# Kernel tuning notes

Measured on AMD Instinct MI355X. Metric: run time of the kernel, lower is better.

The kernel has to match this reference:

```python
import jax, jax.numpy as jnp
import numpy as np

N_TOK, TOKDIM = 2048, 1024
NHEADS, KDIM = 16, 64


def setup_inputs() -> dict:
    key = jax.random.key(0)
    kg, kk, kq = jax.random.split(key, 3)
    g = jax.random.normal(kg, (N_TOK, TOKDIM), dtype=jnp.float32)
    # params use normal(stddev=0.002) init, as in the flax module
    Wk = 0.002 * jax.random.normal(kk, (NHEADS, KDIM, TOKDIM), dtype=jnp.float32)
    Wq = 0.002 * jax.random.normal(kq, (NHEADS, KDIM, TOKDIM), dtype=jnp.float32)
    return {"g": g, "Wk": Wk, "Wq": Wq}


def reference(g, Wk, Wq):
    """manual_grad of the attention energy: returns d(energy)/dg, shape [n, d]."""
    H, Z, D = Wk.shape
    betas = jnp.full((H,), 1.0, dtype=g.dtype) / jnp.sqrt(jnp.asarray(Z, g.dtype))
    K = jnp.einsum('hzd,kd->khz', Wk, g)   # [n,h,z]
    Q = jnp.einsum('hzd,qd->qhz', Wq, g)   # [n,h,z]
    F1 = jnp.einsum('hzd,khz->khd', Wq, K)  # [n,h,d]
    F2 = jnp.einsum('hzd,qhz->qhd', Wk, Q)  # [n,h,d]
    A1 = jnp.einsum('h,khz,qhz->hqk', betas, K, Q)  # [h,q,k] scores
    A2 = jax.nn.softmax(A1, -1)
    T1 = -jnp.einsum('khd,hqk->qd', F1, A2)
    T2 = -jnp.einsum('qhd,hqk->kd', F2, A2)
    return T1 + T2
```

## Files before the change

### kernel.cpp

```cpp
#include <hip/hip_runtime.h>
#include <stdint.h>

#define NT 2048
#define TD 1024
#define NH 16
static constexpr float SCL = 0.18033688011112042f;

typedef __attribute__((ext_vector_type(8))) short bf16x8;
typedef __attribute__((ext_vector_type(4))) float f32x4;
typedef __attribute__((address_space(3))) uint32_t lds_u32;
typedef __attribute__((address_space(1))) uint32_t glb_u32;

__device__ __forceinline__ float bf2f(unsigned short u){
  union { uint32_t u32; float f; } v; v.u32 = ((uint32_t)u) << 16; return v.f;
}
__device__ __forceinline__ unsigned short f2bf(float f){
  union { float f; uint32_t u; } v; v.f = f;
  uint32_t r = v.u + 0x7fffu + ((v.u >> 16) & 1u);
  return (unsigned short)(r >> 16);
}
__device__ __forceinline__ bf16x8 ld8(const unsigned short* base, int row, int kc){
  return *(const bf16x8*)((const char*)base + row*128 + ((kc ^ (row & 7)) << 4));
}
__device__ __forceinline__ bf16x8 ld16(const unsigned short* base, int row, int kc){
  return *(const bf16x8*)((const char*)base + row*256 + ((kc ^ (row & 15)) << 4));
}
template<int N> __device__ __forceinline__ void wait_vm_lgkm0(){
  if constexpr (N == 0)      asm volatile("s_waitcnt vmcnt(0) lgkmcnt(0)" ::: "memory");
  else if constexpr (N == 4) asm volatile("s_waitcnt vmcnt(4) lgkmcnt(0)" ::: "memory");
  else if constexpr (N == 6) asm volatile("s_waitcnt vmcnt(6) lgkmcnt(0)" ::: "memory");
  __builtin_amdgcn_sched_barrier(0);
}

__global__ __launch_bounds__(256) void prep_kernel(
    const float* __restrict__ g, const float* __restrict__ Wk, const float* __restrict__ Wq,
    unsigned short* __restrict__ gbf, unsigned short* __restrict__ wkq,
    unsigned short* __restrict__ twqk)
{
  int b = blockIdx.x;
  if (b < 1024) {
    int base = b * 2048 + threadIdx.x;
    #pragma unroll
    for (int i = 0; i < 8; i++) { int idx = base + i * 256; gbf[idx] = f2bf(g[idx]); }
  } else if (b < 2048) {
    int base = (b - 1024) * 2048 + threadIdx.x;
    #pragma unroll
    for (int i = 0; i < 8; i++) {
      int idx = base + i * 256;
      float v = (idx < (1 << 20)) ? Wk[idx] : Wq[idx - (1 << 20)];
      wkq[idx] = f2bf(v);
    }
  } else {
    int t = b - 2048;
    int dt = t & 31, jt = t >> 5;
    __shared__ float tile[32][33];
    int tx = threadIdx.x & 31, ty = threadIdx.x >> 5;
    int j0 = jt * 32, d0 = dt * 32;
    const float* src = (j0 < 1024) ? Wq : Wk;
    int jb = (j0 < 1024) ? j0 : (j0 - 1024);
    #pragma unroll
    for (int rr = 0; rr < 4; rr++)
      tile[ty + rr * 8][tx] = src[(size_t)(jb + ty + rr * 8) * 1024 + d0 + tx];
    __syncthreads();
    #pragma unroll
    for (int rr = 0; rr < 4; rr++)
      twqk[(size_t)(d0 + ty + rr * 8) * 2048 + j0 + tx] = f2bf(tile[tx][ty + rr * 8]);
  }
}

__global__ __launch_bounds__(256) void qst_kernel(const unsigned short* __restrict__ tkq,
                                                  const float* __restrict__ L,
                                                  unsigned short* __restrict__ qst)
{
  int r = blockIdx.x;
  int h = r >> 6;
  const unsigned short* src = tkq + (size_t)(1024 + r) * 2048;
  unsigned short* dst = qst + (size_t)r * 2048;
  const float* Lh = L + (size_t)h * NT;
  for (int q = threadIdx.x; q < NT; q += 256)
    dst[q] = f2bf(bf2f(src[q]) / Lh[q]);
}

template<int TM, int TN, int EPI>
__global__ __launch_bounds__(256, 2) void btg2_kernel(
    const unsigned short* __restrict__ A, int lda,
    const unsigned short* __restrict__ BT, int ldb,
    int Kdim, void* C0, void* C1)
{
  constexpr int WM = TM / 2, WN = TN / 2, FM = WM / 16, FN = WN / 16;
  constexpr int AC = TM / 32, BC = TN / 32, LOADS = AC + BC;
  __shared__ __align__(16) unsigned short As[3][TM * 64];
  __shared__ __align__(16) unsigned short Bs[3][TN * 64];
  int tid = threadIdx.x, lane = tid & 63, wave = tid >> 6;
  int wr = wave >> 1, wc = wave & 1, lrow = lane & 15, g = lane >> 4;
  int bm = blockIdx.x * TM, bn = blockIdx.y * TN;

  auto stage = [&](unsigned short* bufA, unsigned short* bufB, int kk) {
    #pragma unroll
    for (int i = 0; i < AC; i++) {
      int c = i * 256 + tid, row = c >> 3, sl = ((c & 7) ^ (row & 7)) << 3;
      __builtin_amdgcn_global_load_lds((glb_u32*)(A + (size_t)(bm + row) * lda + kk + sl),
          (lds_u32*)((char*)bufA + i * 4096 + wave * 1024), 16, 0, 0);
    }
    #pragma unroll
    for (int i = 0; i < BC; i++) {
      int c = i * 256 + tid, row = c >> 3, sl = ((c & 7) ^ (row & 7)) << 3;
      __builtin_amdgcn_global_load_lds((glb_u32*)(BT + (size_t)(bn + row) * ldb + kk + sl),
          (lds_u32*)((char*)bufB + i * 4096 + wave * 1024), 16, 0, 0);
    }
  };

  f32x4 acc[FM][FN] = {};
  int nt = Kdim >> 6;
  stage(As[0], Bs[0], 0);
  stage(As[1], Bs[1], 64);
  wait_vm_lgkm0<LOADS>();
  __builtin_amdgcn_s_barrier();
  int bc = 0;
  for (int t = 0; t < nt; t++) {
    int bp = bc + 2; if (bp >= 3) bp -= 3;
    if (t + 2 < nt) stage(As[bp], Bs[bp], (t + 2) * 64);
    const unsigned short* Ac = As[bc];
    const unsigned short* Bc = Bs[bc];
    #pragma unroll
    for (int k2 = 0; k2 < 2; k2++) {
      bf16x8 a_[FM], b_[FN];
      #pragma unroll
      for (int m = 0; m < FM; m++) a_[m] = ld8(Ac, wr * WM + m * 16 + lrow, k2 * 4 + g);
      #pragma unroll
      for (int n = 0; n < FN; n++) b_[n] = ld8(Bc, wc * WN + n * 16 + lrow, k2 * 4 + g);
      #pragma unroll
      for (int m = 0; m < FM; m++)
        #pragma unroll
        for (int n = 0; n < FN; n++)
          acc[m][n] = __builtin_amdgcn_mfma_f32_16x16x32_bf16(a_[m], b_[n], acc[m][n], 0, 0, 0);
    }
    if (t + 2 < nt) wait_vm_lgkm0<LOADS>(); else wait_vm_lgkm0<0>();
    __builtin_amdgcn_s_barrier();
    bc = (bc == 2) ? 0 : bc + 1;
  }
  #pragma unroll
  for (int m = 0; m < FM; m++) {
    int rb = bm + wr * WM + m * 16 + 4 * g;
    #pragma unroll
    for (int n = 0; n < FN; n++) {
      int cc = bn + wc * WN + n * 16 + lrow;
      f32x4 v = acc[m][n];
      if constexpr (EPI == 0) {
        unsigned short* Cp = (unsigned short*)C0;
        unsigned short* T  = (unsigned short*)C1;
        float sc = (bn < 1024) ? SCL : 1.0f;
        unsigned short pt[4];
        #pragma unroll
        for (int j = 0; j < 4; j++) {
          pt[j] = f2bf(v[j]);
          Cp[(size_t)(rb + j) * 2048 + cc] = f2bf(v[j] * sc);
        }
        ushort4 t4; t4.x = pt[0]; t4.y = pt[1]; t4.z = pt[2]; t4.w = pt[3];
        *(ushort4*)(T + (size_t)cc * 2048 + rb) = t4;
      } else {
        float* Cf = (float*)C0;
        #pragma unroll
        for (int j = 0; j < 4; j++) Cf[(size_t)(rb + j) * 1024 + cc] = -v[j];
      }
    }
  }
}

template<bool DIV>
__global__ __launch_bounds__(256, 2) void fused_kernel(
    const unsigned short* __restrict__ CKQ,
    const unsigned short* __restrict__ AUXT,
    unsigned short* __restrict__ C,
    float* __restrict__ Lg)
{
  __shared__ __align__(16) char pool[81920];
  unsigned short* PB = (unsigned short*)(pool + 65536);
  float* Red   = (float*)pool;
  float* L_lds = (float*)(pool + 65536);

  int tid = threadIdx.x, lane = tid & 63, wave = tid >> 6;
  int wr = wave >> 1, wc = wave & 1, lrow = lane & 15, g = lane >> 4;
  int p0 = blockIdx.x * 64, h = blockIdx.y, h64 = h * 64;
  int cA = DIV ? h64 : TD + h64;
  int cB = DIV ? TD + h64 : h64;
  const unsigned short* AuxG = AUXT + (size_t)h64 * 2048;

  auto stageAin = [&](char* dst, int i0) {
    #pragma unroll
    for (int i = 0; i < 4; i++) {
      int c = i * 256 + tid, row = c >> 3, scol = ((c & 7) ^ (row & 7)) << 3;
      __builtin_amdgcn_global_load_lds((glb_u32*)(CKQ + (size_t)(i0 + row) * 2048 + cA + scol),
          (lds_u32*)(dst + i * 4096 + wave * 1024), 16, 0, 0);
    }
  };
  auto stageAux = [&](char* dst, int i0) {
    #pragma unroll
    for (int i = 0; i < 4; i++) {
      int c = i * 256 + tid, row = c >> 4, scol = ((c & 15) ^ (row & 15)) << 3;
      __builtin_amdgcn_global_load_lds((glb_u32*)(AuxG + (size_t)row * 2048 + i0 + scol),
          (lds_u32*)(dst + i * 4096 + wave * 1024), 16, 0, 0);
    }
  };

  #pragma unroll
  for (int i = 0; i < 2; i++) {
    int c = i * 256 + tid, row = c >> 3, scol = ((c & 7) ^ (row & 7)) << 3;
    __builtin_amdgcn_global_load_lds((glb_u32*)(CKQ + (size_t)(p0 + row) * 2048 + cB + scol),
        (lds_u32*)((char*)PB + i * 4096 + wave * 1024), 16, 0, 0);
  }
  stageAin(pool, 0);
  stageAux(pool + 32768, 0);
  wait_vm_lgkm0<0>();
  __builtin_amdgcn_s_barrier();

  bf16x8 bs[2][2];
  #pragma unroll
  for (int k2 = 0; k2 < 2; k2++)
    #pragma unroll
    for (int n = 0; n < 2; n++)
      bs[k2][n] = ld8(PB, wc * 32 + n * 16 + lrow, k2 * 4 + g);
  __syncthreads();

  unsigned short* PldsW = (unsigned short*)(pool + 65536 + wave * 4096);
  f32x4 acc_pv[2][4] = {};
  float lsum[2] = {0.f, 0.f};

  for (int t = 0; t < 16; t++) {
    const unsigned short* curA = (const unsigned short*)(pool + (t & 1) * 16384);
    const unsigned short* curX = (const unsigned short*)(pool + 32768 + (t & 1) * 16384);
    if (t + 1 < 16) {
      stageAin(pool + ((t + 1) & 1) * 16384, (t + 1) * 128);
      stageAux(pool + 32768 + ((t + 1) & 1) * 16384, (t + 1) * 128);
    }
    f32x4 acc_s[4][2] = {};
    __builtin_amdgcn_s_setprio(1);
    #pragma unroll
    for (int k2 = 0; k2 < 2; k2++) {
      bf16x8 a_[4];
      #pragma unroll
      for (int m = 0; m < 4; m++) a_[m] = ld8(curA, wr * 64 + m * 16 + lrow, k2 * 4 + g);
      #pragma unroll
      for (int m = 0; m < 4; m++)
        #pragma unroll
        for (int n = 0; n < 2; n++)
          acc_s[m][n] = __builtin_amdgcn_mfma_f32_16x16x32_bf16(a_[m], bs[k2][n], acc_s[m][n], 0, 0, 0);
    }
    __builtin_amdgcn_s_setprio(0);
    #pragma unroll
    for (int n = 0; n < 2; n++) {
      int pl = n * 16 + lrow;
      #pragma unroll
      for (int m = 0; m < 4; m++) {
        float e0 = exp2f(acc_s[m][n][0]);
        float e1 = exp2f(acc_s[m][n][1]);
        float e2 = exp2f(acc_s[m][n][2]);
        float e3 = exp2f(acc_s[m][n][3]);
        if (DIV) lsum[n] += (e0 + e1) + (e2 + e3);
        uint32_t lo, hi;
        asm("v_cvt_pk_bf16_f32 %0, %1, %2" : "=v"(lo) : "v"(e0), "v"(e1));
        asm("v_cvt_pk_bf16_f32 %0, %1, %2" : "=v"(hi) : "v"(e2), "v"(e3));
        uint2 wv; wv.x = lo; wv.y = hi;
        *(uint2*)((char*)PldsW + pl * 128 + ((((m * 2) + (g >> 1)) ^ (pl & 7)) << 4) + (g & 1) * 8) = wv;
      }
    }
    __builtin_amdgcn_s_setprio(1);
    #pragma unroll
    for (int k2p = 0; k2p < 2; k2p++) {
      bf16x8 pa[2], pb[4];
      #pragma unroll
      for (int m2 = 0; m2 < 2; m2++) pa[m2] = ld8(PldsW, m2 * 16 + lrow, k2p * 4 + g);
      #pragma unroll
      for (int n4 = 0; n4 < 4; n4++) pb[n4] = ld16(curX, n4 * 16 + lrow, wr * 8 + k2p * 4 + g);
      #pragma unroll
      for (int m2 = 0; m2 < 2; m2++)
        #pragma unroll
        for (int n4 = 0; n4 < 4; n4++)
          acc_pv[m2][n4] = __builtin_amdgcn_mfma_f32_16x16x32_bf16(pa[m2], pb[n4], acc_pv[m2][n4], 0, 0, 0);
    }
    __builtin_amdgcn_s_setprio(0);
    wait_vm_lgkm0<0>();
    __builtin_amdgcn_s_barrier();
  }

  #pragma unroll
  for (int m2 = 0; m2 < 2; m2++)
    #pragma unroll
    for (int n4 = 0; n4 < 4; n4++) {
      #pragma unroll
      for (int j = 0; j < 4; j++) {
        int pl = m2 * 16 + 4 * g + j, z = n4 * 16 + lrow;
        Red[(size_t)((wr * 2 + wc) * 32 + pl) * 64 + z] = acc_pv[m2][n4][j];
      }
    }
  if (DIV && tid < 64) L_lds[tid] = 0.f;
  __syncthreads();
  if (DIV) {
    float s0 = lsum[0], s1 = lsum[1];
    s0 += __shfl_xor(s0, 16); s0 += __shfl_xor(s0, 32);
    s1 += __shfl_xor(s1, 16); s1 += __shfl_xor(s1, 32);
    if (lane < 16) {
      atomicAdd(&L_lds[wc * 32 + lrow], s0);
      atomicAdd(&L_lds[wc * 32 + 16 + lrow], s1);
    }
    __syncthreads();
    if (tid < 64) Lg[(size_t)h * NT + p0 + tid] = L_lds[tid];
  }
  int pr = tid >> 2, zb = (tid & 3) * 16;
  int wcr = pr >> 5, pl = pr & 31;
  float inv = (DIV) ? 1.0f / L_lds[pr] : 1.0f;
  int cbase = DIV ? h64 : TD + h64;
  unsigned short ob[16];
  #pragma unroll
  for (int zz = 0; zz < 16; zz += 4) {
    f32x4 s0 = *(f32x4*)&Red[(size_t)((0 * 2 + wcr) * 32 + pl) * 64 + zb + zz];
    f32x4 s1 = *(f32x4*)&Red[(size_t)((1 * 2 + wcr) * 32 + pl) * 64 + zb + zz];
    #pragma unroll
    for (int j = 0; j < 4; j++) ob[zz + j] = f2bf((s0[j] + s1[j]) * inv);
  }
  unsigned short* dst = C + (size_t)(p0 + pr) * 2048 + cbase + zb;
  *(ushort4*)dst = *(ushort4*)&ob[0];
  *(ushort4*)(dst + 4) = *(ushort4*)&ob[4];
  *(ushort4*)(dst + 8) = *(ushort4*)&ob[8];
  *(ushort4*)(dst + 12) = *(ushort4*)&ob[12];
}

extern "C" void kernel_launch(void* const* d_in, const int* in_sizes, int n_in,
                              void* d_out, int out_size, void* d_ws, size_t ws_size,
                              hipStream_t stream)
{
  (void)in_sizes; (void)n_in; (void)out_size; (void)ws_size;
  const float* g  = (const float*)d_in[0];
  const float* Wk = (const float*)d_in[1];
  const float* Wq = (const float*)d_in[2];

  char* ws = (char*)d_ws;
  size_t off = 0;
  auto alloc = [&](size_t b) -> char* {
    char* p = ws + off; off += (b + 255) & ~((size_t)255); return p;
  };
  unsigned short* gbf  = (unsigned short*)alloc((size_t)NT * TD * 2);
  unsigned short* wkq  = (unsigned short*)alloc((size_t)2 * TD * TD * 2);
  unsigned short* twqk = (unsigned short*)alloc((size_t)TD * 2048 * 2);
  unsigned short* CKQ  = (unsigned short*)alloc((size_t)NT * 2048 * 2);
  unsigned short* TKQ  = (unsigned short*)alloc((size_t)NT * 2048 * 2);
  unsigned short* CB12 = (unsigned short*)alloc((size_t)NT * 2048 * 2);
  unsigned short* QsT  = (unsigned short*)alloc((size_t)TD * NT * 2);
  float*          Lbuf = (float*)alloc((size_t)NH * NT * 4);

  prep_kernel<<<dim3(4096), dim3(256), 0, stream>>>(g, Wk, Wq, gbf, wkq, twqk);

  btg2_kernel<128, 64, 0><<<dim3(16, 32), dim3(256), 0, stream>>>(
      gbf, TD, wkq, TD, TD, (void*)CKQ, (void*)TKQ);

  fused_kernel<true><<<dim3(32, NH), dim3(256), 0, stream>>>(CKQ, TKQ, CB12, Lbuf);

  qst_kernel<<<dim3(1024), dim3(256), 0, stream>>>(TKQ, Lbuf, QsT);

  fused_kernel<false><<<dim3(32, NH), dim3(256), 0, stream>>>(CKQ, QsT, CB12, nullptr);

  btg2_kernel<64, 64, 4><<<dim3(32, 16), dim3(256), 0, stream>>>(
      CB12, 2048, twqk, 2048, 2048, d_out, nullptr);
}
```

Before: 122.4 us.

## Split fused attention blocks across eight waves and raise GEMM occupancy bounds

The fused score/softmax/PV kernel now launches 512 threads per block with eight waves instead of four. Each wave owns a 16-column slice of the 64-row P tile instead of 32 columns, which roughly halves its per-wave accumulators and staging loops. The LDS layout, the lsum reduction and the epilogue are reworked to match, and an explicit lgkmcnt wait is placed before the P reload. The final GEMM's launch-bounds occupancy hint is raised from 2 to 3 to cut register use. The aim is more latency hiding per CU, at the cost of extra barrier participants and possible register spills.

```diff
diff --git a/kernel.cpp b/kernel.cpp
--- a/kernel.cpp
+++ b/kernel.cpp
@@ -81,8 +81,8 @@
     dst[q] = f2bf(bf2f(src[q]) / Lh[q]);
 }
 
-template<int TM, int TN, int EPI>
-__global__ __launch_bounds__(256, 2) void btg2_kernel(
+template<int TM, int TN, int EPI, int WPE>
+__global__ __launch_bounds__(256, WPE) void btg2_kernel(
     const unsigned short* __restrict__ A, int lda,
     const unsigned short* __restrict__ BT, int ldb,
     int Kdim, void* C0, void* C1)
@@ -168,7 +168,7 @@
 }
 
 template<bool DIV>
-__global__ __launch_bounds__(256, 2) void fused_kernel(
+__global__ __launch_bounds__(512, 4) void fused_kernel(
     const unsigned short* __restrict__ CKQ,
     const unsigned short* __restrict__ AUXT,
     unsigned short* __restrict__ C,
@@ -177,10 +177,10 @@
   __shared__ __align__(16) char pool[81920];
   unsigned short* PB = (unsigned short*)(pool + 65536);
   float* Red   = (float*)pool;
-  float* L_lds = (float*)(pool + 65536);
+  float* L_lds = (float*)(pool + 32768);
 
   int tid = threadIdx.x, lane = tid & 63, wave = tid >> 6;
-  int wr = wave >> 1, wc = wave & 1, lrow = lane & 15, g = lane >> 4;
+  int wr = wave >> 2, wcq = wave & 3, lrow = lane & 15, g = lane >> 4;
   int p0 = blockIdx.x * 64, h = blockIdx.y, h64 = h * 64;
   int cA = DIV ? h64 : TD + h64;
   int cB = DIV ? TD + h64 : h64;
@@ -188,43 +188,38 @@
 
   auto stageAin = [&](char* dst, int i0) {
     #pragma unroll
-    for (int i = 0; i < 4; i++) {
-      int c = i * 256 + tid, row = c >> 3, scol = ((c & 7) ^ (row & 7)) << 3;
+    for (int i = 0; i < 2; i++) {
+      int c = i * 512 + tid, row = c >> 3, scol = ((c & 7) ^ (row & 7)) << 3;
       __builtin_amdgcn_global_load_lds((glb_u32*)(CKQ + (size_t)(i0 + row) * 2048 + cA + scol),
-          (lds_u32*)(dst + i * 4096 + wave * 1024), 16, 0, 0);
+          (lds_u32*)(dst + i * 8192 + wave * 1024), 16, 0, 0);
     }
   };
   auto stageAux = [&](char* dst, int i0) {
     #pragma unroll
-    for (int i = 0; i < 4; i++) {
-      int c = i * 256 + tid, row = c >> 4, scol = ((c & 15) ^ (row & 15)) << 3;
+    for (int i = 0; i < 2; i++) {
+      int c = i * 512 + tid, row = c >> 4, scol = ((c & 15) ^ (row & 15)) << 3;
       __builtin_amdgcn_global_load_lds((glb_u32*)(AuxG + (size_t)row * 2048 + i0 + scol),
-          (lds_u32*)(dst + i * 4096 + wave * 1024), 16, 0, 0);
+          (lds_u32*)(dst + i * 8192 + wave * 1024), 16, 0, 0);
     }
   };
 
-  #pragma unroll
-  for (int i = 0; i < 2; i++) {
-    int c = i * 256 + tid, row = c >> 3, scol = ((c & 7) ^ (row & 7)) << 3;
+  { int row = tid >> 3, scol = ((tid & 7) ^ (row & 7)) << 3;
     __builtin_amdgcn_global_load_lds((glb_u32*)(CKQ + (size_t)(p0 + row) * 2048 + cB + scol),
-        (lds_u32*)((char*)PB + i * 4096 + wave * 1024), 16, 0, 0);
-  }
+        (lds_u32*)((char*)PB + wave * 1024), 16, 0, 0); }
   stageAin(pool, 0);
   stageAux(pool + 32768, 0);
   wait_vm_lgkm0<0>();
   __builtin_amdgcn_s_barrier();
 
-  bf16x8 bs[2][2];
+  bf16x8 bs[2];
   #pragma unroll
   for (int k2 = 0; k2 < 2; k2++)
-    #pragma unroll
-    for (int n = 0; n < 2; n++)
-      bs[k2][n] = ld8(PB, wc * 32 + n * 16 + lrow, k2 * 4 + g);
+    bs[k2] = ld8(PB, wcq * 16 + lrow, k2 * 4 + g);
   __syncthreads();
 
-  unsigned short* PldsW = (unsigned short*)(pool + 65536 + wave * 4096);
-  f32x4 acc_pv[2][4] = {};
-  float lsum[2] = {0.f, 0.f};
+  unsigned short* PldsW = (unsigned short*)(pool + 65536 + wave * 2048);
+  f32x4 acc_pv[4] = {};
+  float lsum = 0.f;
 
   for (int t = 0; t < 16; t++) {
     const unsigned short* curA = (const unsigned short*)(pool + (t & 1) * 16384);
@@ -233,7 +228,7 @@
       stageAin(pool + ((t + 1) & 1) * 16384, (t + 1) * 128);
       stageAux(pool + 32768 + ((t + 1) & 1) * 16384, (t + 1) * 128);
     }
-    f32x4 acc_s[4][2] = {};
+    f32x4 acc_s[4] = {};
     __builtin_amdgcn_s_setprio(1);
     #pragma unroll
     for (int k2 = 0; k2 < 2; k2++) {
@@ -242,41 +237,34 @@
       for (int m = 0; m < 4; m++) a_[m] = ld8(curA, wr * 64 + m * 16 + lrow, k2 * 4 + g);
       #pragma unroll
       for (int m = 0; m < 4; m++)
-        #pragma unroll
-        for (int n = 0; n < 2; n++)
-          acc_s[m][n] = __builtin_amdgcn_mfma_f32_16x16x32_bf16(a_[m], bs[k2][n], acc_s[m][n], 0, 0, 0);
+        acc_s[m] = __builtin_amdgcn_mfma_f32_16x16x32_bf16(a_[m], bs[k2], acc_s[m], 0, 0, 0);
     }
     __builtin_amdgcn_s_setprio(0);
     #pragma unroll
-    for (int n = 0; n < 2; n++) {
-      int pl = n * 16 + lrow;
-      #pragma unroll
-      for (int m = 0; m < 4; m++) {
-        float e0 = exp2f(acc_s[m][n][0]);
-        float e1 = exp2f(acc_s[m][n][1]);
-        float e2 = exp2f(acc_s[m][n][2]);
-        float e3 = exp2f(acc_s[m][n][3]);
-        if (DIV) lsum[n] += (e0 + e1) + (e2 + e3);
-        uint32_t lo, hi;
-        asm("v_cvt_pk_bf16_f32 %0, %1, %2" : "=v"(lo) : "v"(e0), "v"(e1));
-        asm("v_cvt_pk_bf16_f32 %0, %1, %2" : "=v"(hi) : "v"(e2), "v"(e3));
-        uint2 wv; wv.x = lo; wv.y = hi;
-        *(uint2*)((char*)PldsW + pl * 128 + ((((m * 2) + (g >> 1)) ^ (pl & 7)) << 4) + (g & 1) * 8) = wv;
+    for (int m = 0; m < 4; m++) {
+      float e0 = exp2f(acc_s[m][0]);
+      float e1 = exp2f(acc_s[m][1]);
+      float e2 = exp2f(acc_s[m][2]);
+      float e3 = exp2f(acc_s[m][3]);
+      if (DIV) lsum += (e0 + e1) + (e2 + e3);
+      uint32_t lo, hi;
+      asm("v_cvt_pk_bf16_f32 %0, %1, %2" : "=v"(lo) : "v"(e0), "v"(e1));
+      asm("v_cvt_pk_bf16_f32 %0, %1, %2" : "=v"(hi) : "v"(e2), "v"(e3));
+      uint2 wv; wv.x = lo; wv.y = hi;
+      int slot = m * 2 + (g >> 1);
+      *(uint2*)((char*)PldsW + lrow * 128 + ((slot ^ (lrow & 7)) << 4) + (g & 1) * 8) = wv;
+    }
+    asm volatile("s_waitcnt lgkmcnt(0)" ::: "memory");
+    __builtin_amdgcn_sched_barrier(0);
+    __builtin_amdgcn_s_setprio(1);
+    #pragma unroll
+    for (int k2p = 0; k2p < 2; k2p++) {
+      bf16x8 pa = ld8(PldsW, lrow, k2p * 4 + g);
+      #pragma unroll
+      for (int n4 = 0; n4 < 4; n4++) {
+        bf16x8 pb = ld16(curX, n4 * 16 + lrow, wr * 8 + k2p * 4 + g);
+        acc_pv[n4] = __builtin_amdgcn_mfma_f32_16x16x32_bf16(pa, pb, acc_pv[n4], 0, 0, 0);
       }
-    }
-    __builtin_amdgcn_s_setprio(1);
-    #pragma unroll
-    for (int k2p = 0; k2p < 2; k2p++) {
-      bf16x8 pa[2], pb[4];
-      #pragma unroll
-      for (int m2 = 0; m2 < 2; m2++) pa[m2] = ld8(PldsW, m2 * 16 + lrow, k2p * 4 + g);
-      #pragma unroll
-      for (int n4 = 0; n4 < 4; n4++) pb[n4] = ld16(curX, n4 * 16 + lrow, wr * 8 + k2p * 4 + g);
-      #pragma unroll
-      for (int m2 = 0; m2 < 2; m2++)
-        #pragma unroll
-        for (int n4 = 0; n4 < 4; n4++)
-          acc_pv[m2][n4] = __builtin_amdgcn_mfma_f32_16x16x32_bf16(pa[m2], pb[n4], acc_pv[m2][n4], 0, 0, 0);
     }
     __builtin_amdgcn_s_setprio(0);
     wait_vm_lgkm0<0>();
@@ -284,45 +272,32 @@
   }
 
   #pragma unroll
-  for (int m2 = 0; m2 < 2; m2++)
-    #pragma unroll
-    for (int n4 = 0; n4 < 4; n4++) {
-      #pragma unroll
-      for (int j = 0; j < 4; j++) {
-        int pl = m2 * 16 + 4 * g + j, z = n4 * 16 + lrow;
-        Red[(size_t)((wr * 2 + wc) * 32 + pl) * 64 + z] = acc_pv[m2][n4][j];
-      }
-    }
+  for (int n4 = 0; n4 < 4; n4++)
+    #pragma unroll
+    for (int j = 0; j < 4; j++)
+      Red[(size_t)(wr * 64 + wcq * 16 + 4 * g + j) * 64 + n4 * 16 + lrow] = acc_pv[n4][j];
   if (DIV && tid < 64) L_lds[tid] = 0.f;
   __syncthreads();
   if (DIV) {
-    float s0 = lsum[0], s1 = lsum[1];
-    s0 += __shfl_xor(s0, 16); s0 += __shfl_xor(s0, 32);
-    s1 += __shfl_xor(s1, 16); s1 += __shfl_xor(s1, 32);
-    if (lane < 16) {
-      atomicAdd(&L_lds[wc * 32 + lrow], s0);
-      atomicAdd(&L_lds[wc * 32 + 16 + lrow], s1);
-    }
+    lsum += __shfl_xor(lsum, 16); lsum += __shfl_xor(lsum, 32);
+    if (lane < 16) atomicAdd(&L_lds[wcq * 16 + lane], lsum);
     __syncthreads();
     if (tid < 64) Lg[(size_t)h * NT + p0 + tid] = L_lds[tid];
   }
-  int pr = tid >> 2, zb = (tid & 3) * 16;
-  int wcr = pr >> 5, pl = pr & 31;
-  float inv = (DIV) ? 1.0f / L_lds[pr] : 1.0f;
+  int p = tid >> 3, zb = (tid & 7) * 8;
+  float inv = DIV ? 1.0f / L_lds[p] : 1.0f;
   int cbase = DIV ? h64 : TD + h64;
-  unsigned short ob[16];
+  unsigned short ob[8];
   #pragma unroll
-  for (int zz = 0; zz < 16; zz += 4) {
-    f32x4 s0 = *(f32x4*)&Red[(size_t)((0 * 2 + wcr) * 32 + pl) * 64 + zb + zz];
-    f32x4 s1 = *(f32x4*)&Red[(size_t)((1 * 2 + wcr) * 32 + pl) * 64 + zb + zz];
+  for (int zz = 0; zz < 8; zz += 4) {
+    f32x4 s0 = *(f32x4*)&Red[(size_t)(0 * 64 + p) * 64 + zb + zz];
+    f32x4 s1 = *(f32x4*)&Red[(size_t)(1 * 64 + p) * 64 + zb + zz];
     #pragma unroll
     for (int j = 0; j < 4; j++) ob[zz + j] = f2bf((s0[j] + s1[j]) * inv);
   }
-  unsigned short* dst = C + (size_t)(p0 + pr) * 2048 + cbase + zb;
+  unsigned short* dst = C + (size_t)(p0 + p) * 2048 + cbase + zb;
   *(ushort4*)dst = *(ushort4*)&ob[0];
   *(ushort4*)(dst + 4) = *(ushort4*)&ob[4];
-  *(ushort4*)(dst + 8) = *(ushort4*)&ob[8];
-  *(ushort4*)(dst + 12) = *(ushort4*)&ob[12];
 }
 
 extern "C" void kernel_launch(void* const* d_in, const int* in_sizes, int n_in,
@@ -350,15 +325,15 @@
 
   prep_kernel<<<dim3(4096), dim3(256), 0, stream>>>(g, Wk, Wq, gbf, wkq, twqk);
 
-  btg2_kernel<128, 64, 0><<<dim3(16, 32), dim3(256), 0, stream>>>(
+  btg2_kernel<128, 64, 0, 2><<<dim3(16, 32), dim3(256), 0, stream>>>(
       gbf, TD, wkq, TD, TD, (void*)CKQ, (void*)TKQ);
 
-  fused_kernel<true><<<dim3(32, NH), dim3(256), 0, stream>>>(CKQ, TKQ, CB12, Lbuf);
+  fused_kernel<true><<<dim3(32, NH), dim3(512), 0, stream>>>(CKQ, TKQ, CB12, Lbuf);
 
   qst_kernel<<<dim3(1024), dim3(256), 0, stream>>>(TKQ, Lbuf, QsT);
 
-  fused_kernel<false><<<dim3(32, NH), dim3(256), 0, stream>>>(CKQ, QsT, CB12, nullptr);
-
-  btg2_kernel<64, 64, 4><<<dim3(32, 16), dim3(256), 0, stream>>>(
+  fused_kernel<false><<<dim3(32, NH), dim3(512), 0, stream>>>(CKQ, QsT, CB12, nullptr);
+
+  btg2_kernel<64, 64, 4, 3><<<dim3(32, 16), dim3(256), 0, stream>>>(
       CB12, 2048, twqk, 2048, 2048, d_out, nullptr);
 }
```

New measurement: 120.6 us. About the same (-1.5%).
